# Performance work log

Measured on AMD Instinct MI355X. Metric: run time of the kernel, lower is better.

The kernel has to match this reference:

```python
import jax, jax.numpy as jnp
import numpy as np

MODES = 16
DIM = 16      # comb(modes + photons - 1, photons) with photons=1 -> modes
BATCH = 32768


def _mesh_targets(modes):
    # Full rectangular Clements mesh, 0-indexed mode pairs, modes*(modes-1)/2 elements.
    pairs = []
    for layer in range(modes):
        for i in range(layer % 2, modes - 1, 2):
            pairs.append((i, i + 1))
    return np.asarray(pairs, dtype=np.int32)


def setup_inputs() -> dict:
    key = jax.random.key(0)
    k1, k2, k3 = jax.random.split(key, 3)
    targets = jnp.asarray(_mesh_targets(MODES))  # [120, 2] int32
    E = targets.shape[0]
    params = jax.random.normal(k1, (BATCH, 2 * E), dtype=jnp.float32)
    state_re = jax.random.normal(k2, (BATCH, DIM, DIM), dtype=jnp.float32)
    state_im = jax.random.normal(k3, (BATCH, DIM, DIM), dtype=jnp.float32)
    return {"params": params, "state_re": state_re, "state_im": state_im, "targets": targets}


def _clements_unitary(theta, phi, m_idx, n_idx):
    # Sequentially embed 2x2 MZI blocks T(m,n,theta,phi) into a DIMxDIM unitary:
    # U <- T @ U, where T is identity except rows (m, n):
    #   T[m,m]=e^{i phi} cos th, T[m,n]=-sin th, T[n,m]=e^{i phi} sin th, T[n,n]=cos th
    # Only two rows of U change per step, so we update rows instead of a full matmul.
    U0 = jnp.eye(DIM, dtype=jnp.complex64)

    def step(U, x):
        mi, ni, t, p = x
        c = jnp.cos(t)
        s = jnp.sin(t)
        e = jnp.exp(1j * p)  # complex64
        rm = U[mi]
        rn = U[ni]
        U = U.at[mi].set(e * c * rm - s * rn)
        U = U.at[ni].set(e * s * rm + c * rn)
        return U, None

    U, _ = jax.lax.scan(step, U0, (m_idx, n_idx, theta, phi))
    # diag phases are all zero in UParamLayer.map_clements -> identity, skipped.
    return U


def reference(params, state_re, state_im, targets):
    E = targets.shape[0]
    theta = params[:, :E]          # [B, E]
    phi = params[:, E:2 * E]       # [B, E]
    m_idx = targets[:, 0]
    n_idx = targets[:, 1]

    U = jax.vmap(lambda t, p: _clements_unitary(t, p, m_idx, n_idx))(theta, phi)  # [B, D, D] c64
    rho = jax.lax.complex(state_re, state_im)  # [B, D, D] c64

    left = jnp.einsum('bij,bjk->bik', U, rho)             # U @ rho
    out = jnp.einsum('bik,bjk->bij', left, jnp.conj(U))   # (U @ rho) @ U^dagger
    # Return real/imag stacked so the baseline output is a plain float tensor.
    return jnp.stack([out.real, out.imag], axis=1)  # [B, 2, D, D] f32
```

## Files before the change

### kernel.cpp

```cpp
#include <hip/hip_runtime.h>

#define DIM 16
#define NE 120
#define ITEMS 8
#define THREADS 128
#define USTRIDE 20
#define UITEM 640
#define LDS_FLOATS (ITEMS * UITEM)

typedef float v2f __attribute__((ext_vector_type(2)));


__global__ __launch_bounds__(THREADS, 2) void uparam_kernel(
    const float* __restrict__ params,
    const float* __restrict__ state_re,
    const float* __restrict__ state_im,
    float* __restrict__ out)
{
    __shared__ float lds[LDS_FLOATS];

    const int tid  = threadIdx.x;
    const int item = tid >> 4;
    const int r    = tid & 15;
    const long b   = (long)blockIdx.x * ITEMS + item;

    float* slot = lds + item * UITEM;
    float* cst  = slot + 8 * (item & 3);

    {
        const float* prow = params + b * (2 * NE);
        #pragma unroll
        for (int k = 0; k < 15; ++k) {
            const int a = k * 16 + r;
            float s, c;
            __sincosf(prow[a], &s, &c);
            const int e   = (a < NE) ? a : a - NE;
            const int off = (a < NE) ? 0 : 2;
            *(float2*)(cst + 4 * e + off) = make_float2(c, s);
        }
    }
    __syncthreads();

    float Ur[DIM], Ui[DIM];
    #pragma unroll
    for (int i = 0; i < DIM; ++i) { Ur[i] = (i == r) ? 1.0f : 0.0f; Ui[i] = 0.0f; }

    #pragma unroll 1
    for (int l2 = 0; l2 < 8; ++l2) {
        const int eb = l2 * 15;
        #pragma unroll
        for (int j = 0; j < 15; ++j) {
            const int m = (j < 8) ? 2 * j : 2 * (j - 8) + 1;
            const int n = m + 1;
            const float4 cs = *(const float4*)(cst + 4 * (eb + j));
            const float c = cs.x, s = cs.y, cp = cs.z, sp = cs.w;
            const float rmr = Ur[m], rmi = Ui[m], rnr = Ur[n], rni = Ui[n];
            const float wr = cp * rmr - sp * rmi;
            const float wi = cp * rmi + sp * rmr;
            Ur[m] = c * wr - s * rnr;
            Ui[m] = c * wi - s * rni;
            Ur[n] = s * wr + c * rnr;
            Ui[n] = s * wi + c * rni;
        }
    }

    __syncthreads();

    #pragma unroll
    for (int i = 0; i < DIM; ++i) {
        slot[i * USTRIDE + r] = Ur[i];
        slot[DIM * USTRIDE + i * USTRIDE + r] = Ui[i];
    }
    __syncthreads();

    v2f Lr2[8], Li2[8];
    #pragma unroll
    for (int k = 0; k < 8; ++k) { Lr2[k] = (v2f)(0.0f); Li2[k] = (v2f)(0.0f); }

    const float4* rhor = (const float4*)(state_re + b * (DIM * DIM));
    const float4* rhoi = (const float4*)(state_im + b * (DIM * DIM));
    const float* Urow_r = slot + r * USTRIDE;
    const float* Urow_i = slot + DIM * USTRIDE + r * USTRIDE;

    #pragma unroll 1
    for (int j4 = 0; j4 < 4; ++j4) {
        const float4 u4r = *(const float4*)(Urow_r + j4 * 4);
        const float4 u4i = *(const float4*)(Urow_i + j4 * 4);
        const float uar[4] = { u4r.x, u4r.y, u4r.z, u4r.w };
        const float uai[4] = { u4i.x, u4i.y, u4i.z, u4i.w };
        #pragma unroll
        for (int jj = 0; jj < 4; ++jj) {
            const int j = j4 * 4 + jj;
            const v2f ur2 = { uar[jj], uar[jj] };
            const v2f ui2 = { uai[jj], uai[jj] };
            #pragma unroll
            for (int k4 = 0; k4 < 4; ++k4) {
                const float4 pr = rhor[j * 4 + k4];
                const float4 pi = rhoi[j * 4 + k4];
                const v2f pr0 = { pr.x, pr.y }, pr1 = { pr.z, pr.w };
                const v2f pi0 = { pi.x, pi.y }, pi1 = { pi.z, pi.w };
                Lr2[2*k4+0] = Lr2[2*k4+0] + ur2 * pr0 - ui2 * pi0;
                Lr2[2*k4+1] = Lr2[2*k4+1] + ur2 * pr1 - ui2 * pi1;
                Li2[2*k4+0] = Li2[2*k4+0] + ur2 * pi0 + ui2 * pr0;
                Li2[2*k4+1] = Li2[2*k4+1] + ur2 * pi1 + ui2 * pr1;
            }
        }
    }

    float* outp = out + b * (2 * DIM * DIM) + r * DIM;
    #pragma unroll 1
    for (int jj = 0; jj < 4; ++jj) {
        float orr[4], oii[4];
        #pragma unroll
        for (int j4 = 0; j4 < 4; ++j4) {
            const int j = jj * 4 + j4;
            const float* Uj_r = slot + j * USTRIDE;
            const float* Uj_i = slot + DIM * USTRIDE + j * USTRIDE;
            v2f ar2 = (v2f)(0.0f), ai2 = (v2f)(0.0f);
            #pragma unroll
            for (int k4 = 0; k4 < 4; ++k4) {
                const float4 ur4 = *(const float4*)(Uj_r + k4 * 4);
                const float4 ui4 = *(const float4*)(Uj_i + k4 * 4);
                const v2f ur0 = { ur4.x, ur4.y }, ur1 = { ur4.z, ur4.w };
                const v2f ui0 = { ui4.x, ui4.y }, ui1 = { ui4.z, ui4.w };
                ar2 = ar2 + Lr2[2*k4+0] * ur0 + Li2[2*k4+0] * ui0;
                ar2 = ar2 + Lr2[2*k4+1] * ur1 + Li2[2*k4+1] * ui1;
                ai2 = ai2 + Li2[2*k4+0] * ur0 - Lr2[2*k4+0] * ui0;
                ai2 = ai2 + Li2[2*k4+1] * ur1 - Lr2[2*k4+1] * ui1;
            }
            orr[j4] = ar2.x + ar2.y;
            oii[j4] = ai2.x + ai2.y;
        }
        *(float4*)(outp + jj * 4) = make_float4(orr[0], orr[1], orr[2], orr[3]);
        *(float4*)(outp + DIM * DIM + jj * 4) = make_float4(oii[0], oii[1], oii[2], oii[3]);
    }
}

extern "C" void kernel_launch(void* const* d_in, const int* in_sizes, int n_in,
                              void* d_out, int out_size, void* d_ws, size_t ws_size,
                              hipStream_t stream) {
    const float* params   = (const float*)d_in[0];
    const float* state_re = (const float*)d_in[1];
    const float* state_im = (const float*)d_in[2];
    float* out = (float*)d_out;

    const int batch = in_sizes[0] / (2 * NE);
    dim3 grid(batch / ITEMS);
    uparam_kernel<<<grid, THREADS, 0, stream>>>(params, state_re, state_im, out);
}
```

Measured before the change: 78.49 us.

## Double-buffer rho row loads and shrink blocks to one wavefront

Shrinks the block to a single 64-thread wavefront of 4 items and pads the per-item LDS slot. The first rho row is prefetched before the MZI chain so its load latency hides behind the rotation work. The U·rho loop then ping-pongs between two register buffers, loading the next row while the current one is accumulated. The MZI update is rewritten with packed complex vectors. Register pressure goes up, and smaller blocks change how blocks are scheduled and how many fit per CU.

```diff
diff --git a/kernel.cpp b/kernel.cpp
--- a/kernel.cpp
+++ b/kernel.cpp
@@ -2,10 +2,10 @@
 
 #define DIM 16
 #define NE 120
-#define ITEMS 8
-#define THREADS 128
+#define ITEMS 4
+#define THREADS 64
 #define USTRIDE 20
-#define UITEM 640
+#define UITEM 648
 #define LDS_FLOATS (ITEMS * UITEM)
 
 typedef float v2f __attribute__((ext_vector_type(2)));
@@ -25,7 +25,6 @@
     const long b   = (long)blockIdx.x * ITEMS + item;
 
     float* slot = lds + item * UITEM;
-    float* cst  = slot + 8 * (item & 3);
 
     {
         const float* prow = params + b * (2 * NE);
@@ -36,14 +35,21 @@
             __sincosf(prow[a], &s, &c);
             const int e   = (a < NE) ? a : a - NE;
             const int off = (a < NE) ? 0 : 2;
-            *(float2*)(cst + 4 * e + off) = make_float2(c, s);
+            *(float2*)(slot + 4 * e + off) = make_float2(c, s);
         }
     }
+
+    const float4* rhor = (const float4*)(state_re + b * (DIM * DIM));
+    const float4* rhoi = (const float4*)(state_im + b * (DIM * DIM));
+
+    float4 Ar0 = rhor[0], Ar1 = rhor[1], Ar2 = rhor[2], Ar3 = rhor[3];
+    float4 Ai0 = rhoi[0], Ai1 = rhoi[1], Ai2 = rhoi[2], Ai3 = rhoi[3];
+
     __syncthreads();
 
-    float Ur[DIM], Ui[DIM];
+    v2f Uv[DIM];
     #pragma unroll
-    for (int i = 0; i < DIM; ++i) { Ur[i] = (i == r) ? 1.0f : 0.0f; Ui[i] = 0.0f; }
+    for (int i = 0; i < DIM; ++i) Uv[i] = (v2f){ (i == r) ? 1.0f : 0.0f, 0.0f };
 
     #pragma unroll 1
     for (int l2 = 0; l2 < 8; ++l2) {
@@ -52,24 +58,21 @@
         for (int j = 0; j < 15; ++j) {
             const int m = (j < 8) ? 2 * j : 2 * (j - 8) + 1;
             const int n = m + 1;
-            const float4 cs = *(const float4*)(cst + 4 * (eb + j));
+            const float4 cs = *(const float4*)(slot + 4 * (eb + j));
             const float c = cs.x, s = cs.y, cp = cs.z, sp = cs.w;
-            const float rmr = Ur[m], rmi = Ui[m], rnr = Ur[n], rni = Ui[n];
-            const float wr = cp * rmr - sp * rmi;
-            const float wi = cp * rmi + sp * rmr;
-            Ur[m] = c * wr - s * rnr;
-            Ui[m] = c * wi - s * rni;
-            Ur[n] = s * wr + c * rnr;
-            Ui[n] = s * wi + c * rni;
+            const v2f um = Uv[m], un = Uv[n];
+            const v2f jm = { -um.y, um.x };
+            const v2f w  = cp * um + sp * jm;
+            Uv[m] = c * w - s * un;
+            Uv[n] = s * w + c * un;
         }
     }
-
     __syncthreads();
 
     #pragma unroll
     for (int i = 0; i < DIM; ++i) {
-        slot[i * USTRIDE + r] = Ur[i];
-        slot[DIM * USTRIDE + i * USTRIDE + r] = Ui[i];
+        slot[i * USTRIDE + r] = Uv[i].x;
+        slot[DIM * USTRIDE + i * USTRIDE + r] = Uv[i].y;
     }
     __syncthreads();
 
@@ -77,35 +80,64 @@
     #pragma unroll
     for (int k = 0; k < 8; ++k) { Lr2[k] = (v2f)(0.0f); Li2[k] = (v2f)(0.0f); }
 
-    const float4* rhor = (const float4*)(state_re + b * (DIM * DIM));
-    const float4* rhoi = (const float4*)(state_im + b * (DIM * DIM));
     const float* Urow_r = slot + r * USTRIDE;
     const float* Urow_i = slot + DIM * USTRIDE + r * USTRIDE;
 
+    float4 Br0, Br1, Br2, Br3, Bi0, Bi1, Bi2, Bi3;
+
+#define LOADA(J) do { Ar0=rhor[(J)*4]; Ar1=rhor[(J)*4+1]; Ar2=rhor[(J)*4+2]; Ar3=rhor[(J)*4+3]; \
+                      Ai0=rhoi[(J)*4]; Ai1=rhoi[(J)*4+1]; Ai2=rhoi[(J)*4+2]; Ai3=rhoi[(J)*4+3]; } while(0)
+#define LOADB(J) do { Br0=rhor[(J)*4]; Br1=rhor[(J)*4+1]; Br2=rhor[(J)*4+2]; Br3=rhor[(J)*4+3]; \
+                      Bi0=rhoi[(J)*4]; Bi1=rhoi[(J)*4+1]; Bi2=rhoi[(J)*4+2]; Bi3=rhoi[(J)*4+3]; } while(0)
+
+    auto upd = [&](const float4 R0, const float4 R1, const float4 R2, const float4 R3,
+                   const float4 I0, const float4 I1, const float4 I2, const float4 I3,
+                   const float ur, const float ui) {
+        const v2f u_r = { ur, ur }, u_i = { ui, ui };
+        Lr2[0] += u_r * (v2f){R0.x, R0.y} - u_i * (v2f){I0.x, I0.y};
+        Lr2[1] += u_r * (v2f){R0.z, R0.w} - u_i * (v2f){I0.z, I0.w};
+        Lr2[2] += u_r * (v2f){R1.x, R1.y} - u_i * (v2f){I1.x, I1.y};
+        Lr2[3] += u_r * (v2f){R1.z, R1.w} - u_i * (v2f){I1.z, I1.w};
+        Lr2[4] += u_r * (v2f){R2.x, R2.y} - u_i * (v2f){I2.x, I2.y};
+        Lr2[5] += u_r * (v2f){R2.z, R2.w} - u_i * (v2f){I2.z, I2.w};
+        Lr2[6] += u_r * (v2f){R3.x, R3.y} - u_i * (v2f){I3.x, I3.y};
+        Lr2[7] += u_r * (v2f){R3.z, R3.w} - u_i * (v2f){I3.z, I3.w};
+        Li2[0] += u_r * (v2f){I0.x, I0.y} + u_i * (v2f){R0.x, R0.y};
+        Li2[1] += u_r * (v2f){I0.z, I0.w} + u_i * (v2f){R0.z, R0.w};
+        Li2[2] += u_r * (v2f){I1.x, I1.y} + u_i * (v2f){R1.x, R1.y};
+        Li2[3] += u_r * (v2f){I1.z, I1.w} + u_i * (v2f){R1.z, R1.w};
+        Li2[4] += u_r * (v2f){I2.x, I2.y} + u_i * (v2f){R2.x, R2.y};
+        Li2[5] += u_r * (v2f){I2.z, I2.w} + u_i * (v2f){R2.z, R2.w};
+        Li2[6] += u_r * (v2f){I3.x, I3.y} + u_i * (v2f){R3.x, R3.y};
+        Li2[7] += u_r * (v2f){I3.z, I3.w} + u_i * (v2f){R3.z, R3.w};
+    };
+
     #pragma unroll 1
-    for (int j4 = 0; j4 < 4; ++j4) {
-        const float4 u4r = *(const float4*)(Urow_r + j4 * 4);
-        const float4 u4i = *(const float4*)(Urow_i + j4 * 4);
-        const float uar[4] = { u4r.x, u4r.y, u4r.z, u4r.w };
-        const float uai[4] = { u4i.x, u4i.y, u4i.z, u4i.w };
-        #pragma unroll
-        for (int jj = 0; jj < 4; ++jj) {
-            const int j = j4 * 4 + jj;
-            const v2f ur2 = { uar[jj], uar[jj] };
-            const v2f ui2 = { uai[jj], uai[jj] };
-            #pragma unroll
-            for (int k4 = 0; k4 < 4; ++k4) {
-                const float4 pr = rhor[j * 4 + k4];
-                const float4 pi = rhoi[j * 4 + k4];
-                const v2f pr0 = { pr.x, pr.y }, pr1 = { pr.z, pr.w };
-                const v2f pi0 = { pi.x, pi.y }, pi1 = { pi.z, pi.w };
-                Lr2[2*k4+0] = Lr2[2*k4+0] + ur2 * pr0 - ui2 * pi0;
-                Lr2[2*k4+1] = Lr2[2*k4+1] + ur2 * pr1 - ui2 * pi1;
-                Li2[2*k4+0] = Li2[2*k4+0] + ur2 * pi0 + ui2 * pr0;
-                Li2[2*k4+1] = Li2[2*k4+1] + ur2 * pi1 + ui2 * pr1;
-            }
-        }
+    for (int j4 = 0; j4 < 3; ++j4) {
+        const float4 u4r = *(const float4*)(Urow_r + 4 * j4);
+        const float4 u4i = *(const float4*)(Urow_i + 4 * j4);
+        LOADB(4 * j4 + 1);
+        upd(Ar0, Ar1, Ar2, Ar3, Ai0, Ai1, Ai2, Ai3, u4r.x, u4i.x);
+        LOADA(4 * j4 + 2);
+        upd(Br0, Br1, Br2, Br3, Bi0, Bi1, Bi2, Bi3, u4r.y, u4i.y);
+        LOADB(4 * j4 + 3);
+        upd(Ar0, Ar1, Ar2, Ar3, Ai0, Ai1, Ai2, Ai3, u4r.z, u4i.z);
+        LOADA(4 * j4 + 4);
+        upd(Br0, Br1, Br2, Br3, Bi0, Bi1, Bi2, Bi3, u4r.w, u4i.w);
     }
+    {
+        const float4 u4r = *(const float4*)(Urow_r + 12);
+        const float4 u4i = *(const float4*)(Urow_i + 12);
+        LOADB(13);
+        upd(Ar0, Ar1, Ar2, Ar3, Ai0, Ai1, Ai2, Ai3, u4r.x, u4i.x);
+        LOADA(14);
+        upd(Br0, Br1, Br2, Br3, Bi0, Bi1, Bi2, Bi3, u4r.y, u4i.y);
+        LOADB(15);
+        upd(Ar0, Ar1, Ar2, Ar3, Ai0, Ai1, Ai2, Ai3, u4r.z, u4i.z);
+        upd(Br0, Br1, Br2, Br3, Bi0, Bi1, Bi2, Bi3, u4r.w, u4i.w);
+    }
+#undef LOADA
+#undef LOADB
 
     float* outp = out + b * (2 * DIM * DIM) + r * DIM;
     #pragma unroll 1
```

Result: faster. 65.43 us (-16.6%).
